# Kernel tuning notes

Hardware: AMD Instinct MI355X
Metric: run time of the kernel (lower is better)

The kernel has to match this reference:

```python
import jax, jax.numpy as jnp
import numpy as np

B, L, D = 2, 2048, 1024
H = 16
HD = D // H  # 64


def setup_inputs() -> dict:
    key = jax.random.key(0)
    k1, k2, k3, k4 = jax.random.split(key, 4)
    s = 0.02
    x = jax.random.normal(k1, (B, L, D), dtype=jnp.float32)
    qkv_w = jax.random.normal(k2, (3 * D, D), dtype=jnp.float32) * s
    out_w = jax.random.normal(k3, (D, D), dtype=jnp.float32) * s
    out_b = jax.random.normal(k4, (D,), dtype=jnp.float32) * s
    return {"x": x, "qkv_w": qkv_w, "out_w": out_w, "out_b": out_b}


def reference(x, qkv_w, out_w, out_b):
    b, l, d = x.shape
    # qkv projection (no bias): [B,L,3D] -> [3,B,H,L,HD]
    qkv = jnp.einsum('bld,ed->ble', x, qkv_w)
    qkv = qkv.reshape(b, l, 3, H, HD).transpose(2, 0, 3, 1, 4)
    q, k, v = qkv[0], qkv[1], qkv[2]
    # scaled dot-product scores [B,H,L,L]
    scores = jnp.einsum('bhqd,bhkd->bhqk', q, k) / jnp.sqrt(jnp.float32(HD))
    causal_mask = jnp.triu(jnp.ones((l, l), dtype=bool), k=1)
    scores = jnp.where(causal_mask, -jnp.inf, scores)
    probs = jax.nn.softmax(scores, axis=-1)
    # dropout is identity in eval / p=0
    out = jnp.einsum('bhqk,bhkd->bhqd', probs, v)
    out = out.transpose(0, 2, 1, 3).reshape(b, l, d)
    return out @ out_w.T + out_b
```

## Files before the change

### kernel.cpp

```cpp
#include <hip/hip_runtime.h>
#include <hip/hip_bf16.h>
#include <cstdint>


typedef __attribute__((ext_vector_type(8))) short sh8;
typedef __attribute__((ext_vector_type(4))) short sh4;
typedef __attribute__((ext_vector_type(4))) float f32x4;

__device__ __forceinline__ unsigned short f2b(float f) {
  unsigned int u = __float_as_uint(f);
  u += 0x7FFFu + ((u >> 16) & 1u);
  return (unsigned short)(u >> 16);
}

__device__ __forceinline__ unsigned int pack2(float lo, float hi) {
  return (unsigned int)f2b(lo) | ((unsigned int)f2b(hi) << 16);
}

__device__ __forceinline__ f32x4 mfma16x16x16(sh4 a, sh4 b, f32x4 c) {
#if __has_builtin(__builtin_amdgcn_mfma_f32_16x16x16bf16_1k)
  return __builtin_amdgcn_mfma_f32_16x16x16bf16_1k(a, b, c, 0, 0, 0);
#else
  asm volatile("v_mfma_f32_16x16x16_bf16 %0, %1, %2, %0" : "+v"(c) : "v"(a), "v"(b));
  return c;
#endif
}

__device__ __forceinline__ void gload_lds16(const void* g, void* l) {
  __builtin_amdgcn_global_load_lds((__attribute__((address_space(1))) void*)g,
                                   (__attribute__((address_space(3))) void*)l,
                                   16, 0, 0);
}

__global__ __launch_bounds__(256) void k_cvt(const float* __restrict__ in,
                                             unsigned short* __restrict__ out, int n) {
  int idx = (blockIdx.x * 256 + threadIdx.x) * 4;
  if (idx >= n) return;
  float4 v = *(const float4*)&in[idx];
  union { unsigned short u[4]; uint2 w; } r;
  r.u[0] = f2b(v.x); r.u[1] = f2b(v.y); r.u[2] = f2b(v.z); r.u[3] = f2b(v.w);
  *(uint2*)&out[idx] = r.w;
}

template<int MT, int NT>
__device__ __forceinline__ void gemm_bt_core(
    const unsigned short* __restrict__ A,
    const unsigned short* __restrict__ B,
    int K, int m0, int n0,
    unsigned short* ldsA, unsigned short* ldsB,
    f32x4 acc[MT][NT]) {
  constexpr int TA = MT * 32 / 32;
  constexpr int TB = NT * 32 / 32;
  const int tid  = threadIdx.x;
  const int wv   = tid >> 6;
  const int lane = tid & 63;
  const int wm = (wv >> 1) * (MT * 16);
  const int wn = (wv & 1) * (NT * 16);
  const int fr = lane & 15;
  const int g  = lane >> 4;

  for (int k0 = 0; k0 < K; k0 += 64) {
#pragma unroll
    for (int t = 0; t < TA; ++t) {
      int gi = t * 256 + tid;
      int r = gi >> 3, c = gi & 7;
      gload_lds16(&A[(size_t)(m0 + r) * K + k0 + ((c ^ (r & 7)) << 3)], &ldsA[gi * 8]);
    }
#pragma unroll
    for (int t = 0; t < TB; ++t) {
      int gi = t * 256 + tid;
      int r = gi >> 3, c = gi & 7;
      gload_lds16(&B[(size_t)(n0 + r) * K + k0 + ((c ^ (r & 7)) << 3)], &ldsB[gi * 8]);
    }
    __syncthreads();
#pragma unroll
    for (int ks = 0; ks < 2; ++ks) {
      sh8 af[MT], bf[NT];
#pragma unroll
      for (int mt = 0; mt < MT; ++mt)
        af[mt] = *(const sh8*)&ldsA[(wm + mt * 16 + fr) * 64 +
                                    ((((ks << 2) + g) ^ (fr & 7)) << 3)];
#pragma unroll
      for (int nt = 0; nt < NT; ++nt)
        bf[nt] = *(const sh8*)&ldsB[(wn + nt * 16 + fr) * 64 +
                                    ((((ks << 2) + g) ^ (fr & 7)) << 3)];
#pragma unroll
      for (int mt = 0; mt < MT; ++mt)
#pragma unroll
        for (int nt = 0; nt < NT; ++nt)
          acc[mt][nt] = __builtin_amdgcn_mfma_f32_16x16x32_bf16(af[mt], bf[nt], acc[mt][nt], 0, 0, 0);
    }
    __syncthreads();
  }
}

__global__ __launch_bounds__(256, 5) void k_qkv_gemm(
    const unsigned short* __restrict__ xb, const unsigned short* __restrict__ wq,
    unsigned short* __restrict__ Q, unsigned short* __restrict__ Kc,
    unsigned short* __restrict__ Vt) {
  __shared__ __align__(16) unsigned short ldsA[64 * 64];
  __shared__ __align__(16) unsigned short ldsB[128 * 64];
  f32x4 acc[2][4];
  const f32x4 fz = {0.f, 0.f, 0.f, 0.f};
#pragma unroll
  for (int i = 0; i < 2; ++i)
#pragma unroll
    for (int j = 0; j < 4; ++j) acc[i][j] = fz;

  const int m0 = blockIdx.x * 64, n0 = blockIdx.y * 128;
  gemm_bt_core<2, 4>(xb, wq, 1024, m0, n0, ldsA, ldsB, acc);

  const int tid = threadIdx.x, wv = tid >> 6, lane = tid & 63;
  const int wm = (wv >> 1) << 5, wn = (wv & 1) << 6;
  const int r4 = (lane >> 4) << 2, fr = lane & 15;
#pragma unroll
  for (int mt = 0; mt < 2; ++mt)
#pragma unroll
    for (int nt = 0; nt < 4; ++nt) {
      const int row0 = m0 + wm + mt * 16 + r4;
      const int col  = n0 + wn + nt * 16 + fr;
      const int b = row0 >> 11;
      const int which = col >> 10, rem = col & 1023;
      const int h = rem >> 6, hd = rem & 63;
      const size_t bh = (size_t)(b * 16 + h);
      if (which == 2) {
        const size_t vb = (bh * 64 + hd) * 2048 + (row0 & 2047);
        *(unsigned int*)&Vt[vb]     = pack2(acc[mt][nt][0], acc[mt][nt][1]);
        *(unsigned int*)&Vt[vb + 2] = pack2(acc[mt][nt][2], acc[mt][nt][3]);
      } else {
#pragma unroll
        for (int i = 0; i < 4; ++i) {
          const int lq = (row0 + i) & 2047;
          float v = acc[mt][nt][i];
          if (which == 0) Q [(bh * 2048 + lq) * 64 + hd] = f2b(v * 0.125f);
          else            Kc[(bh * 2048 + lq) * 64 + hd] = f2b(v);
        }
      }
    }
}

__global__ __launch_bounds__(256, 4) void k_attn(
    const unsigned short* __restrict__ Q, const unsigned short* __restrict__ Kc,
    const unsigned short* __restrict__ Vt, unsigned short* __restrict__ attn) {
  __shared__ __align__(16) unsigned short kbuf[2][32 * 64];
  __shared__ __align__(16) unsigned short vbuf[2][64 * 32];

  const int bh  = blockIdx.x & 31;
  const int grp = 31 - (blockIdx.x >> 5);
  const int wv = threadIdx.x >> 6, lane = threadIdx.x & 63;
  const int tid = threadIdx.x;
  const int strip = (grp << 2) + wv;
  const int qw = strip << 4;
  const int b = bh >> 4, h = bh & 15;
  const unsigned short* Qb = Q  + (size_t)bh * 2048 * 64;
  const unsigned short* Kb = Kc + (size_t)bh * 2048 * 64;
  const unsigned short* Vb = Vt + (size_t)bh * 64 * 2048;
  const int fr = lane & 15, g = lane >> 4;
  const int fk = g << 3, r4 = g << 2;
  const f32x4 fz = {0.f, 0.f, 0.f, 0.f};
  const int vswz = (fr & 3) ^ ((fr >> 2) & 3);

  const int ksrow = tid >> 3, kslog = (tid & 7) ^ (ksrow & 7);
  const int vsrow = tid >> 2, vslog = (tid & 3) ^ ((vsrow & 3) ^ ((vsrow >> 2) & 3));

  sh8 qf[2];
#pragma unroll
  for (int ks = 0; ks < 2; ++ks)
    qf[ks] = *(const sh8*)&Qb[(size_t)(qw + fr) * 64 + ks * 32 + fk];

  f32x4 o[4];
#pragma unroll
  for (int i = 0; i < 4; ++i) o[i] = fz;
  float m_i = -1e30f, lp = 0.f;

  const int njw = (qw + 47) >> 5;
  const int njm = ((grp << 6) + 95) >> 5;

  gload_lds16(&Kb[(size_t)ksrow * 64 + kslog * 8], &kbuf[0][tid * 8]);
  gload_lds16(&Vb[(size_t)vsrow * 2048 + vslog * 8], &vbuf[0][tid * 8]);

  for (int j = 0; j < njm; ++j) {
    __syncthreads();
    if (j + 1 < njm) {
      const int kvn = (j + 1) << 5;
      const int nb = (j + 1) & 1;
      gload_lds16(&Kb[(size_t)(kvn + ksrow) * 64 + kslog * 8], &kbuf[nb][tid * 8]);
      gload_lds16(&Vb[(size_t)vsrow * 2048 + kvn + vslog * 8], &vbuf[nb][tid * 8]);
    }
    if (j < njw) {
      const int kvb = j << 5;
      const unsigned short* kb = kbuf[j & 1];
      const unsigned short* vb = vbuf[j & 1];
      f32x4 s[2]; s[0] = fz; s[1] = fz;
#pragma unroll
      for (int t = 0; t < 2; ++t)
#pragma unroll
        for (int ks = 0; ks < 2; ++ks) {
          sh8 kf = *(const sh8*)&kb[(t * 16 + fr) * 64 + ((((ks << 2) + g) ^ (fr & 7)) << 3)];
          s[t] = __builtin_amdgcn_mfma_f32_16x16x32_bf16(kf, qf[ks], s[t], 0, 0, 0);
        }
      sh4 vf[4][2];
#pragma unroll
      for (int hb = 0; hb < 4; ++hb)
#pragma unroll
        for (int t = 0; t < 2; ++t)
          vf[hb][t] = *(const sh4*)&vb[(hb * 16 + fr) * 32 +
                                       ((((t << 1) + (g >> 1)) ^ vswz) << 3) + ((g & 1) << 2)];

      if (j == njw - 1) {
#pragma unroll
        for (int t = 0; t < 2; ++t)
#pragma unroll
          for (int i = 0; i < 4; ++i)
            if (kvb + t * 16 + r4 + i > qw + fr) s[t][i] = -1e30f;
      }
      float pm = fmaxf(fmaxf(fmaxf(s[0][0], s[0][1]), fmaxf(s[0][2], s[0][3])),
                       fmaxf(fmaxf(s[1][0], s[1][1]), fmaxf(s[1][2], s[1][3])));
      if (!__all(pm - m_i <= 8.0f)) {
        float rm = fmaxf(pm, __shfl_xor(pm, 16, 64));
        rm = fmaxf(rm, __shfl_xor(rm, 32, 64));
        const float mn = fmaxf(m_i, rm);
        const float sc = __expf(m_i - mn);
        m_i = mn;
        lp *= sc;
#pragma unroll
        for (int hb = 0; hb < 4; ++hb)
#pragma unroll
          for (int i = 0; i < 4; ++i) o[hb][i] *= sc;
      }
      float p0[4], p1[4];
#pragma unroll
      for (int i = 0; i < 4; ++i) {
        p0[i] = __expf(s[0][i] - m_i);
        p1[i] = __expf(s[1][i] - m_i);
      }
      lp += ((p0[0] + p0[1]) + (p0[2] + p0[3])) + ((p1[0] + p1[1]) + (p1[2] + p1[3]));

      union { unsigned int w[2]; sh4 v; } pb0, pb1;
      pb0.w[0] = pack2(p0[0], p0[1]); pb0.w[1] = pack2(p0[2], p0[3]);
      pb1.w[0] = pack2(p1[0], p1[1]); pb1.w[1] = pack2(p1[2], p1[3]);
#pragma unroll
      for (int hb = 0; hb < 4; ++hb) {
        o[hb] = mfma16x16x16(vf[hb][0], pb0.v, o[hb]);
        o[hb] = mfma16x16x16(vf[hb][1], pb1.v, o[hb]);
      }
    }
  }

  float l = lp;
  l += __shfl_xor(l, 16, 64);
  l += __shfl_xor(l, 32, 64);
  const float inv = 1.0f / l;
  const size_t base = ((size_t)(b * 2048 + qw + fr)) * 1024 + h * 64;
#pragma unroll
  for (int hb = 0; hb < 4; ++hb)
#pragma unroll
    for (int i2 = 0; i2 < 2; ++i2) {
      unsigned int pw = pack2(o[hb][2 * i2] * inv, o[hb][2 * i2 + 1] * inv);
      *(unsigned int*)&attn[base + hb * 16 + r4 + 2 * i2] = pw;
    }
}

__global__ __launch_bounds__(256, 5) void k_out_gemm(
    const unsigned short* __restrict__ attn, const unsigned short* __restrict__ wo,
    const float* __restrict__ bias, float* __restrict__ out) {
  __shared__ __align__(16) unsigned short ldsA[64 * 64];
  __shared__ __align__(16) unsigned short ldsB[64 * 64];
  f32x4 acc[2][2];
  const f32x4 fz = {0.f, 0.f, 0.f, 0.f};
#pragma unroll
  for (int i = 0; i < 2; ++i)
#pragma unroll
    for (int j = 0; j < 2; ++j) acc[i][j] = fz;

  const int m0 = blockIdx.x * 64, n0 = blockIdx.y * 64;
  gemm_bt_core<2, 2>(attn, wo, 1024, m0, n0, ldsA, ldsB, acc);

  const int tid = threadIdx.x, wv = tid >> 6, lane = tid & 63;
  const int wm = (wv >> 1) << 5, wn = (wv & 1) << 5;
  const int r4 = (lane >> 4) << 2, fr = lane & 15;
#pragma unroll
  for (int mt = 0; mt < 2; ++mt)
#pragma unroll
    for (int nt = 0; nt < 2; ++nt)
#pragma unroll
      for (int i = 0; i < 4; ++i) {
        int row = m0 + wm + mt * 16 + r4 + i;
        int col = n0 + wn + nt * 16 + fr;
        out[(size_t)row * 1024 + col] = acc[mt][nt][i] + bias[col];
      }
}

extern "C" void kernel_launch(void* const* d_in, const int* in_sizes, int n_in,
                              void* d_out, int out_size, void* d_ws, size_t ws_size,
                              hipStream_t stream) {
  const float* x     = (const float*)d_in[0];
  const float* qkv_w = (const float*)d_in[1];
  const float* out_w = (const float*)d_in[2];
  const float* out_b = (const float*)d_in[3];
  float* out = (float*)d_out;

  unsigned short* ws   = (unsigned short*)d_ws;
  unsigned short* xb   = ws;
  unsigned short* wq   = xb  + 4096 * 1024;
  unsigned short* wo   = wq  + 3072 * 1024;
  unsigned short* Qs   = wo  + 1024 * 1024;
  unsigned short* Ks   = Qs  + 32 * 2048 * 64;
  unsigned short* Vts  = Ks  + 32 * 2048 * 64;
  unsigned short* attn = Vts + 32 * 64 * 2048;

  k_cvt<<<4096, 256, 0, stream>>>(x,     xb, 4096 * 1024);
  k_cvt<<<3072, 256, 0, stream>>>(qkv_w, wq, 3072 * 1024);
  k_cvt<<<1024, 256, 0, stream>>>(out_w, wo, 1024 * 1024);
  k_qkv_gemm<<<dim3(64, 24), 256, 0, stream>>>(xb, wq, Qs, Ks, Vts);
  k_attn<<<1024, 256, 0, stream>>>(Qs, Ks, Vts, attn);
  k_out_gemm<<<dim3(64, 16), 256, 0, stream>>>(attn, wo, out_b, out);
}
```

Baseline: 117.0 us.

## Enlarge attention KV tile to 64 and make all waves share the loop

Each iteration of the flash-attention inner loop now processes a 64-key K/V tile instead of 32. This halves the number of barrier and prefetch rounds, and the causal mask is applied only on the final tile. The per-wave early-exit (njw) is removed, so all four waves now run the same trip count. LDS double buffers grow to 64x64 with an 8-way XOR swizzle, and V fragments are loaded per tile inside the PV loop. The cost is more LDS per block, which may reduce occupancy, plus some wasted masked work for waves whose diagonal falls earlier in the tile.

```diff
diff --git a/kernel.cpp b/kernel.cpp
--- a/kernel.cpp
+++ b/kernel.cpp
@@ -49,8 +49,8 @@
     int K, int m0, int n0,
     unsigned short* ldsA, unsigned short* ldsB,
     f32x4 acc[MT][NT]) {
-  constexpr int TA = MT * 32 / 32;
-  constexpr int TB = NT * 32 / 32;
+  constexpr int TA = MT;
+  constexpr int TB = NT;
   const int tid  = threadIdx.x;
   const int wv   = tid >> 6;
   const int lane = tid & 63;
@@ -142,8 +142,8 @@
 __global__ __launch_bounds__(256, 4) void k_attn(
     const unsigned short* __restrict__ Q, const unsigned short* __restrict__ Kc,
     const unsigned short* __restrict__ Vt, unsigned short* __restrict__ attn) {
-  __shared__ __align__(16) unsigned short kbuf[2][32 * 64];
-  __shared__ __align__(16) unsigned short vbuf[2][64 * 32];
+  __shared__ __align__(16) unsigned short kbuf[2][64 * 64];
+  __shared__ __align__(16) unsigned short vbuf[2][64 * 64];
 
   const int bh  = blockIdx.x & 31;
   const int grp = 31 - (blockIdx.x >> 5);
@@ -158,10 +158,9 @@
   const int fr = lane & 15, g = lane >> 4;
   const int fk = g << 3, r4 = g << 2;
   const f32x4 fz = {0.f, 0.f, 0.f, 0.f};
-  const int vswz = (fr & 3) ^ ((fr >> 2) & 3);
-
-  const int ksrow = tid >> 3, kslog = (tid & 7) ^ (ksrow & 7);
-  const int vsrow = tid >> 2, vslog = (tid & 3) ^ ((vsrow & 3) ^ ((vsrow >> 2) & 3));
+
+  const int sgr0 = tid >> 3,        sgc0 = tid & 7;
+  const int sgr1 = (tid + 256) >> 3, sgc1 = tid & 7;
 
   sh8 qf[2];
 #pragma unroll
@@ -173,76 +172,77 @@
   for (int i = 0; i < 4; ++i) o[i] = fz;
   float m_i = -1e30f, lp = 0.f;
 
-  const int njw = (qw + 47) >> 5;
-  const int njm = ((grp << 6) + 95) >> 5;
-
-  gload_lds16(&Kb[(size_t)ksrow * 64 + kslog * 8], &kbuf[0][tid * 8]);
-  gload_lds16(&Vb[(size_t)vsrow * 2048 + vslog * 8], &vbuf[0][tid * 8]);
+  const int njm = grp + 1;
+
+  gload_lds16(&Kb[(size_t)sgr0 * 64 + ((sgc0 ^ (sgr0 & 7)) << 3)], &kbuf[0][tid * 8]);
+  gload_lds16(&Kb[(size_t)sgr1 * 64 + ((sgc1 ^ (sgr1 & 7)) << 3)], &kbuf[0][(tid + 256) * 8]);
+  gload_lds16(&Vb[(size_t)sgr0 * 2048 + ((sgc0 ^ (sgr0 & 7)) << 3)], &vbuf[0][tid * 8]);
+  gload_lds16(&Vb[(size_t)sgr1 * 2048 + ((sgc1 ^ (sgr1 & 7)) << 3)], &vbuf[0][(tid + 256) * 8]);
 
   for (int j = 0; j < njm; ++j) {
     __syncthreads();
     if (j + 1 < njm) {
-      const int kvn = (j + 1) << 5;
+      const int kvn = (j + 1) << 6;
       const int nb = (j + 1) & 1;
-      gload_lds16(&Kb[(size_t)(kvn + ksrow) * 64 + kslog * 8], &kbuf[nb][tid * 8]);
-      gload_lds16(&Vb[(size_t)vsrow * 2048 + kvn + vslog * 8], &vbuf[nb][tid * 8]);
-    }
-    if (j < njw) {
-      const int kvb = j << 5;
-      const unsigned short* kb = kbuf[j & 1];
-      const unsigned short* vb = vbuf[j & 1];
-      f32x4 s[2]; s[0] = fz; s[1] = fz;
-#pragma unroll
-      for (int t = 0; t < 2; ++t)
-#pragma unroll
-        for (int ks = 0; ks < 2; ++ks) {
-          sh8 kf = *(const sh8*)&kb[(t * 16 + fr) * 64 + ((((ks << 2) + g) ^ (fr & 7)) << 3)];
-          s[t] = __builtin_amdgcn_mfma_f32_16x16x32_bf16(kf, qf[ks], s[t], 0, 0, 0);
-        }
-      sh4 vf[4][2];
+      gload_lds16(&Kb[(size_t)(kvn + sgr0) * 64 + ((sgc0 ^ (sgr0 & 7)) << 3)], &kbuf[nb][tid * 8]);
+      gload_lds16(&Kb[(size_t)(kvn + sgr1) * 64 + ((sgc1 ^ (sgr1 & 7)) << 3)], &kbuf[nb][(tid + 256) * 8]);
+      gload_lds16(&Vb[(size_t)sgr0 * 2048 + kvn + ((sgc0 ^ (sgr0 & 7)) << 3)], &vbuf[nb][tid * 8]);
+      gload_lds16(&Vb[(size_t)sgr1 * 2048 + kvn + ((sgc1 ^ (sgr1 & 7)) << 3)], &vbuf[nb][(tid + 256) * 8]);
+    }
+    const int kvb = j << 6;
+    const unsigned short* kb = kbuf[j & 1];
+    const unsigned short* vb = vbuf[j & 1];
+    f32x4 s[4];
+#pragma unroll
+    for (int t = 0; t < 4; ++t) s[t] = fz;
+#pragma unroll
+    for (int ks = 0; ks < 2; ++ks)
+#pragma unroll
+      for (int t = 0; t < 4; ++t) {
+        sh8 kf = *(const sh8*)&kb[(t * 16 + fr) * 64 + ((((ks << 2) + g) ^ (fr & 7)) << 3)];
+        s[t] = __builtin_amdgcn_mfma_f32_16x16x32_bf16(kf, qf[ks], s[t], 0, 0, 0);
+      }
+
+    if (j == njm - 1) {
+#pragma unroll
+      for (int t = 0; t < 4; ++t)
+#pragma unroll
+        for (int i = 0; i < 4; ++i)
+          if (kvb + t * 16 + r4 + i > qw + fr) s[t][i] = -1e30f;
+    }
+    float pm = s[0][0];
+#pragma unroll
+    for (int t = 0; t < 4; ++t)
+#pragma unroll
+      for (int i = 0; i < 4; ++i) pm = fmaxf(pm, s[t][i]);
+    if (!__all(pm - m_i <= 8.0f)) {
+      float rm = fmaxf(pm, __shfl_xor(pm, 16, 64));
+      rm = fmaxf(rm, __shfl_xor(rm, 32, 64));
+      const float mn = fmaxf(m_i, rm);
+      const float sc = __expf(m_i - mn);
+      m_i = mn;
+      lp *= sc;
 #pragma unroll
       for (int hb = 0; hb < 4; ++hb)
 #pragma unroll
-        for (int t = 0; t < 2; ++t)
-          vf[hb][t] = *(const sh4*)&vb[(hb * 16 + fr) * 32 +
-                                       ((((t << 1) + (g >> 1)) ^ vswz) << 3) + ((g & 1) << 2)];
-
-      if (j == njw - 1) {
-#pragma unroll
-        for (int t = 0; t < 2; ++t)
-#pragma unroll
-          for (int i = 0; i < 4; ++i)
-            if (kvb + t * 16 + r4 + i > qw + fr) s[t][i] = -1e30f;
-      }
-      float pm = fmaxf(fmaxf(fmaxf(s[0][0], s[0][1]), fmaxf(s[0][2], s[0][3])),
-                       fmaxf(fmaxf(s[1][0], s[1][1]), fmaxf(s[1][2], s[1][3])));
-      if (!__all(pm - m_i <= 8.0f)) {
-        float rm = fmaxf(pm, __shfl_xor(pm, 16, 64));
-        rm = fmaxf(rm, __shfl_xor(rm, 32, 64));
-        const float mn = fmaxf(m_i, rm);
-        const float sc = __expf(m_i - mn);
-        m_i = mn;
-        lp *= sc;
-#pragma unroll
-        for (int hb = 0; hb < 4; ++hb)
-#pragma unroll
-          for (int i = 0; i < 4; ++i) o[hb][i] *= sc;
-      }
-      float p0[4], p1[4];
-#pragma unroll
-      for (int i = 0; i < 4; ++i) {
-        p0[i] = __expf(s[0][i] - m_i);
-        p1[i] = __expf(s[1][i] - m_i);
-      }
-      lp += ((p0[0] + p0[1]) + (p0[2] + p0[3])) + ((p1[0] + p1[1]) + (p1[2] + p1[3]));
-
-      union { unsigned int w[2]; sh4 v; } pb0, pb1;
-      pb0.w[0] = pack2(p0[0], p0[1]); pb0.w[1] = pack2(p0[2], p0[3]);
-      pb1.w[0] = pack2(p1[0], p1[1]); pb1.w[1] = pack2(p1[2], p1[3]);
+        for (int i = 0; i < 4; ++i) o[hb][i] *= sc;
+    }
+#pragma unroll
+    for (int t = 0; t < 4; ++t) {
+#pragma unroll
+      for (int i = 0; i < 4; ++i) s[t][i] = __expf(s[t][i] - m_i);
+      lp += (s[t][0] + s[t][1]) + (s[t][2] + s[t][3]);
+    }
+#pragma unroll
+    for (int t = 0; t < 4; ++t) {
+      union { unsigned int w[2]; sh4 v; } pb;
+      pb.w[0] = pack2(s[t][0], s[t][1]);
+      pb.w[1] = pack2(s[t][2], s[t][3]);
 #pragma unroll
       for (int hb = 0; hb < 4; ++hb) {
-        o[hb] = mfma16x16x16(vf[hb][0], pb0.v, o[hb]);
-        o[hb] = mfma16x16x16(vf[hb][1], pb1.v, o[hb]);
+        sh4 vf = *(const sh4*)&vb[(hb * 16 + fr) * 64 +
+                                  ((((t << 1) + (g >> 1)) ^ (fr & 7)) << 3) + ((g & 1) << 2)];
+        o[hb] = mfma16x16x16(vf, pb.v, o[hb]);
       }
     }
   }
```

New measurement: 106.5 us. 1.1x faster.
